# Kernel optimization log

Measured on AMD Instinct MI355X. Metric: run time of the kernel, lower is better.

Reference implementation:

```python
import jax, jax.numpy as jnp
import numpy as np
import math

B, N, CS, CZ, H, C, P, PV, NB = 1, 512, 384, 128, 12, 16, 4, 8, 64


def quat_to_rot(q):
    q = q / jnp.clip(jnp.linalg.norm(q, axis=-1, keepdims=True), 1e-8)
    w, x, y, z = q[..., 0], q[..., 1], q[..., 2], q[..., 3]
    return jnp.stack([
        w*w + x*x - y*y - z*z, 2*(x*y - w*z), 2*(x*z + w*y),
        2*(x*y + w*z), w*w - x*x + y*y - z*z, 2*(y*z - w*x),
        2*(x*z - w*y), 2*(y*z + w*x), w*w - x*x - y*y + z*z,
    ], axis=-1).reshape(q.shape[:-1] + (3, 3))


def setup_inputs() -> dict:
    key = jax.random.key(0)
    ks = jax.random.split(key, 28)
    def n(k, shape, sc=1.0):
        return jax.random.normal(k, shape, jnp.float32) * sc
    s = n(ks[0], (B, N, CS))
    z = n(ks[1], (B, N, N, CZ))
    translations = n(ks[2], (B, N, 3)) * 4.0  # spread distances over 0-32A bins
    rotations = quat_to_rot(n(ks[3], (B, N, 4)))  # valid SO(3) frames
    mask = jnp.ones((B, N), dtype=bool)
    inv = lambda fan: 1.0 / math.sqrt(fan)
    return {
        's': s, 'z': z, 'translations': translations, 'rotations': rotations, 'mask': mask,
        'Wq': n(ks[4], (CS, H*C), inv(CS)), 'bq': n(ks[5], (H*C,), 0.01),
        'Wk': n(ks[6], (CS, H*C), inv(CS)), 'bk': n(ks[7], (H*C,), 0.01),
        'Wv': n(ks[8], (CS, H*C), inv(CS)), 'bv': n(ks[9], (H*C,), 0.01),
        'Wqp': n(ks[10], (CS, H*P*3), inv(CS)), 'bqp': n(ks[11], (H*P*3,), 0.01),
        'Wkp': n(ks[12], (CS, H*P*3), inv(CS)), 'bkp': n(ks[13], (H*P*3,), 0.01),
        'Wvp': n(ks[14], (CS, H*PV*3), inv(CS)), 'bvp': n(ks[15], (H*PV*3,), 0.01),
        'Wb': n(ks[16], (CZ, H), inv(CZ)), 'bb': n(ks[17], (H,), 0.01),
        'dist_emb': n(ks[18], (NB, H), 0.02),
        'scale_logits': n(ks[19], (3, H), 0.1),
        'head_weights': jnp.abs(n(ks[20], (H,))) * 0.2 + 0.8,
        'Wout': n(ks[21], (H*(C + PV*4 + CZ), CS), inv(H*(C + PV*4 + CZ))),
        'bout': n(ks[22], (CS,), 0.01),
    }


def reference(s, z, translations, rotations, mask, Wq, bq, Wk, bk, Wv, bv,
              Wqp, bqp, Wkp, bkp, Wvp, bvp, Wb, bb, dist_emb, scale_logits,
              head_weights, Wout, bout):
    b, n, _ = s.shape
    q = (s @ Wq + bq).reshape(b, n, H, C)
    k = (s @ Wk + bk).reshape(b, n, H, C)
    v = (s @ Wv + bv).reshape(b, n, H, C)
    q_pts = (s @ Wqp + bqp).reshape(b, n, H, P, 3)
    k_pts = (s @ Wkp + bkp).reshape(b, n, H, P, 3)
    v_pts = (s @ Wvp + bvp).reshape(b, n, H, PV, 3)
    t = translations[:, :, None, None, :]
    q_g = jnp.einsum('bnij,bnhpj->bnhpi', rotations, q_pts) + t
    k_g = jnp.einsum('bnij,bnhpj->bnhpi', rotations, k_pts) + t
    v_g = jnp.einsum('bnij,bnhpj->bnhpi', rotations, v_pts) + t
    scalar_logits = jnp.einsum('bnhc,bmhc->bnmh', q, k) / math.sqrt(C)
    # squared point distances, summed over points p and coords i, via expansion
    q_sq = (q_g**2).sum((-1, -2))  # (b, n, h)
    k_sq = (k_g**2).sum((-1, -2))
    cross = jnp.einsum('bnhpi,bmhpi->bnmh', q_g, k_g)
    point_dist = q_sq[:, :, None, :] + k_sq[:, None, :, :] - 2.0 * cross
    point_logits = -0.5 * point_dist * head_weights
    pair_bias = z @ Wb + bb  # (b, n, m, h)
    pair_dist = jnp.linalg.norm(
        translations[:, :, None, :] - translations[:, None, :, :], axis=-1)
    edges = jnp.linspace(0.0, 32.0, NB + 1)
    bins = jnp.clip(jnp.searchsorted(edges, pair_dist, side='left') - 1, 0, NB - 1)
    dist_bias = dist_emb[bins]
    local = (pair_dist <= 5.0).astype(s.dtype)
    medium = ((pair_dist > 5.0) & (pair_dist <= 15.0)).astype(s.dtype)
    scales = jnp.stack([local, medium, jnp.ones_like(pair_dist)], axis=-1)
    per_head = jax.nn.softmax(scale_logits, axis=0)  # (3, h)
    multiscale = jnp.einsum('bnms,sh->bnmh', scales, per_head)
    logits = scalar_logits + point_logits + pair_bias + dist_bias + multiscale
    m2d = mask[:, :, None] & mask[:, None, :]
    logits = jnp.where(m2d[..., None], logits, -10000.0)
    attn = jax.nn.softmax(logits.astype(jnp.float32), axis=2).astype(s.dtype)
    out_scalar = jnp.einsum('bnmh,bmhc->bnhc', attn, v)
    out_pts_g = jnp.einsum('bnmh,bmhpi->bnhpi', attn, v_g)
    out_pts_l = jnp.einsum('bnji,bnhpj->bnhpi', rotations, out_pts_g - t)  # R^T x
    out_norms = jnp.linalg.norm(out_pts_l, axis=-1)  # (b, n, h, pv)
    pair_feat = jnp.einsum('bnmh,bnmc->bnhc', attn, z)
    feats = jnp.concatenate(
        [out_scalar, out_pts_l.reshape(b, n, H, PV * 3), out_norms, pair_feat],
        axis=-1).reshape(b, n, -1)
    return feats @ Wout + bout
```

## Files before the change

kernel.cpp:

```cpp
#include <hip/hip_runtime.h>
#include <math.h>

#define N   512
#define CS  384
#define CZ  128
#define H   12
#define C   16
#define P   4
#define PV  8
#define NB  64
#define KSP 528
#define QKD 28
#define QPAD 68
#define APAD 516

#define OFF_Q    0
#define OFF_K    98304
#define OFF_V    196608
#define OFF_QP   294912
#define OFF_KP   368640
#define OFF_VP   442368
#define OFF_QG   589824
#define OFF_KG   663552
#define OFF_VG   737280
#define OFF_QSQ  884736
#define OFF_KSQ  890880
#define OFF_LOG  897024
#define OFF_FEAT 4042752

__global__ __launch_bounds__(256) void k_proj(
    const float* __restrict__ s,
    const float* __restrict__ Wq,  const float* __restrict__ bq,
    const float* __restrict__ Wk,  const float* __restrict__ bk,
    const float* __restrict__ Wv,  const float* __restrict__ bv,
    const float* __restrict__ Wqp, const float* __restrict__ bqp,
    const float* __restrict__ Wkp, const float* __restrict__ bkp,
    const float* __restrict__ Wvp, const float* __restrict__ bvp,
    float* __restrict__ ws)
{
    __shared__ float s_s[16*388];
    __shared__ float part[4*16*68];
    const int tid = threadIdx.x;
    const int n0  = blockIdx.y * 16;
    const int cq  = tid & 15;
    const int rg  = (tid >> 4) & 3;
    const int ks  = tid >> 6;
    const int gc  = blockIdx.x * 64 + cq * 4;
    for (int i = tid; i < 16*384; i += 256) {
        int r = i / 384, c = i - r*384;
        s_s[r*388 + c] = s[(n0 + r)*384 + c];
    }
    __syncthreads();
    const float* W; int width; int lc;
    if      (gc < 192) { W=Wq;  width=192; lc=gc;     }
    else if (gc < 384) { W=Wk;  width=192; lc=gc-192; }
    else if (gc < 576) { W=Wv;  width=192; lc=gc-384; }
    else if (gc < 720) { W=Wqp; width=144; lc=gc-576; }
    else if (gc < 864) { W=Wkp; width=144; lc=gc-720; }
    else               { W=Wvp; width=288; lc=gc-864; }
    float acc[4][4] = {{0.f}};
    const float* wp   = W + lc + (size_t)(ks*96)*width;
    const float* srow = s_s + (rg*4)*388 + ks*96;
    #pragma unroll 4
    for (int kk = 0; kk < 96; kk++) {
        float4 w4 = *(const float4*)(wp + (size_t)kk*width);
        #pragma unroll
        for (int r = 0; r < 4; r++) {
            float sv = srow[r*388 + kk];
            acc[r][0] += sv*w4.x; acc[r][1] += sv*w4.y;
            acc[r][2] += sv*w4.z; acc[r][3] += sv*w4.w;
        }
    }
    #pragma unroll
    for (int r = 0; r < 4; r++)
        *(float4*)(part + (ks*16 + rg*4 + r)*68 + cq*4) =
            make_float4(acc[r][0], acc[r][1], acc[r][2], acc[r][3]);
    __syncthreads();
    {
        const int row = tid >> 4;
        float4 sum = *(const float4*)(part + (0*16 + row)*68 + cq*4);
        #pragma unroll
        for (int k2 = 1; k2 < 4; k2++) {
            float4 p = *(const float4*)(part + (k2*16 + row)*68 + cq*4);
            sum.x += p.x; sum.y += p.y; sum.z += p.z; sum.w += p.w;
        }
        const float* b; float* dst; int w2, lc2;
        if      (gc < 192) { b=bq;  w2=192; lc2=gc;     dst=ws+OFF_Q;  }
        else if (gc < 384) { b=bk;  w2=192; lc2=gc-192; dst=ws+OFF_K;  }
        else if (gc < 576) { b=bv;  w2=192; lc2=gc-384; dst=ws+OFF_V;  }
        else if (gc < 720) { b=bqp; w2=144; lc2=gc-576; dst=ws+OFF_QP; }
        else if (gc < 864) { b=bkp; w2=144; lc2=gc-720; dst=ws+OFF_KP; }
        else               { b=bvp; w2=288; lc2=gc-864; dst=ws+OFF_VP; }
        float4 b4 = *(const float4*)(b + lc2);
        sum.x += b4.x; sum.y += b4.y; sum.z += b4.z; sum.w += b4.w;
        *(float4*)(dst + (size_t)(n0+row)*w2 + lc2) = sum;
    }
}

__global__ __launch_bounds__(192) void k_frames(
    const float* __restrict__ rot, const float* __restrict__ trans,
    float* __restrict__ ws)
{
    int n = blockIdx.x, tid = threadIdx.x;
    __shared__ float R[9], T[3], qg_s[144], kg_s[144];
    if (tid < 9) R[tid] = rot[n*9 + tid];
    if (tid < 3) T[tid] = trans[n*3 + tid];
    __syncthreads();
    if (tid < 48) {
        const float* lp = ws + OFF_QP + n*144 + tid*3;
        float l0=lp[0], l1=lp[1], l2=lp[2];
        float* gp = ws + OFF_QG + n*144 + tid*3;
        for (int i=0;i<3;i++){ float g = R[i*3+0]*l0 + R[i*3+1]*l1 + R[i*3+2]*l2 + T[i]; gp[i]=g; qg_s[tid*3+i]=g; }
    } else if (tid < 96) {
        int u = tid-48;
        const float* lp = ws + OFF_KP + n*144 + u*3;
        float l0=lp[0], l1=lp[1], l2=lp[2];
        float* gp = ws + OFF_KG + n*144 + u*3;
        for (int i=0;i<3;i++){ float g = R[i*3+0]*l0 + R[i*3+1]*l1 + R[i*3+2]*l2 + T[i]; gp[i]=g; kg_s[u*3+i]=g; }
    } else {
        int u = tid-96;
        const float* lp = ws + OFF_VP + n*288 + u*3;
        float l0=lp[0], l1=lp[1], l2=lp[2];
        float* gp = ws + OFF_VG + n*288 + u*3;
        for (int i=0;i<3;i++){ float g = R[i*3+0]*l0 + R[i*3+1]*l1 + R[i*3+2]*l2 + T[i]; gp[i]=g; }
    }
    __syncthreads();
    if (tid < 12) {
        float a=0;
        for (int d=0; d<12; d++){ float x=qg_s[tid*12+d]; a+=x*x; }
        ws[OFF_QSQ + n*12 + tid]=a;
    } else if (tid < 24) {
        int h = tid-12; float a=0;
        for (int d=0; d<12; d++){ float x=kg_s[h*12+d]; a+=x*x; }
        ws[OFF_KSQ + n*12 + h]=a;
    }
}

__global__ __launch_bounds__(256) void k_qkpt(
    const float* __restrict__ head_weights, float* __restrict__ ws)
{
    __shared__ float qs[QKD*QPAD], ks[QKD*QPAD], qa[64], kb[64];
    const int tid = threadIdx.x;
    const int m0 = blockIdx.x * 64, n0 = blockIdx.y * 64, h = blockIdx.z;
    const float hw = head_weights[h];
    for (int idx = tid; idx < 64*16; idx += 256) {
        int r = idx >> 4, c = idx & 15;
        qs[c*QPAD + r] = ws[OFF_Q + (n0+r)*192 + h*16 + c] * 0.25f;
        ks[c*QPAD + r] = ws[OFF_K + (m0+r)*192 + h*16 + c];
    }
    for (int idx = tid; idx < 64*12; idx += 256) {
        int r = idx / 12, c = idx % 12;
        qs[(16+c)*QPAD + r] = ws[OFF_QG + (n0+r)*144 + h*12 + c] * hw;
        ks[(16+c)*QPAD + r] = ws[OFF_KG + (m0+r)*144 + h*12 + c];
    }
    for (int idx = tid; idx < 64; idx += 256) {
        qa[idx] = -0.5f * hw * ws[OFF_QSQ + (n0+idx)*12 + h];
        kb[idx] = -0.5f * hw * ws[OFF_KSQ + (m0+idx)*12 + h];
    }
    __syncthreads();
    const int tx = tid & 15, ty = tid >> 4;
    float acc[4][4] = {{0.f}};
    #pragma unroll 4
    for (int d = 0; d < QKD; d++) {
        float4 a = *(const float4*)(qs + d*QPAD + ty*4);
        float4 b = *(const float4*)(ks + d*QPAD + tx*4);
        const float* ap = &a.x; const float* bp = &b.x;
        #pragma unroll
        for (int i=0;i<4;i++)
            #pragma unroll
            for (int j=0;j<4;j++) acc[i][j] += ap[i]*bp[j];
    }
    #pragma unroll
    for (int i=0;i<4;i++) {
        float ai = qa[ty*4+i];
        float4 r;
        r.x = acc[i][0] + ai + kb[tx*4+0];
        r.y = acc[i][1] + ai + kb[tx*4+1];
        r.z = acc[i][2] + ai + kb[tx*4+2];
        r.w = acc[i][3] + ai + kb[tx*4+3];
        *(float4*)(ws + OFF_LOG + ((size_t)(n0+ty*4+i)*H + h)*N + m0 + tx*4) = r;
    }
}

__global__ __launch_bounds__(256) void k_attn_all(
    const float* __restrict__ z, const float* __restrict__ trans,
    const float* __restrict__ rot,
    const float* __restrict__ Wb, const float* __restrict__ bb,
    const float* __restrict__ dist_emb, const float* __restrict__ scale_logits,
    float* __restrict__ ws)
{
    __shared__ float attn_s[H*APAD];
    __shared__ float part[4*12*64];
    __shared__ float og_s[288];
    __shared__ float sprob[36];
    const int n = blockIdx.x, tid = threadIdx.x;
    const int lane = tid & 63, wave = tid >> 6;

    if (tid < 12) {
        float sa = scale_logits[tid], sb = scale_logits[12+tid], sc = scale_logits[24+tid];
        float mx = fmaxf(sa, fmaxf(sb, sc));
        float ea=__expf(sa-mx), eb=__expf(sb-mx), ec=__expf(sc-mx);
        float inv = 1.f/(ea+eb+ec);
        sprob[tid] = ea*inv; sprob[12+tid] = eb*inv; sprob[24+tid] = ec*inv;
    }

    const float4* asrc = (const float4*)(ws + OFF_LOG + (size_t)n*H*N);
    for (int i = tid; i < H*(N/4); i += 256) {
        int h = i >> 7, q = i & 127;
        *(float4*)(attn_s + h*APAD + q*4) = asrc[h*128 + q];
    }
    __syncthreads();

    const float tnx = trans[n*3+0], tny = trans[n*3+1], tnz = trans[n*3+2];
    const float4 bb0 = *(const float4*)(bb);
    const float4 bb1 = *(const float4*)(bb+4);
    const float4 bb2 = *(const float4*)(bb+8);
    for (int half = 0; half < 2; half++) {
        const int m = tid + half*256;
        float dx = tnx - trans[m*3+0];
        float dy = tny - trans[m*3+1];
        float dz = tnz - trans[m*3+2];
        float pd = sqrtf(dx*dx+dy*dy+dz*dz);
        int bin = (int)ceilf(2.f*pd) - 1;
        bin = bin < 0 ? 0 : (bin > NB-1 ? NB-1 : bin);
        const float4 de0 = *(const float4*)(dist_emb + bin*12);
        const float4 de1 = *(const float4*)(dist_emb + bin*12 + 4);
        const float4 de2 = *(const float4*)(dist_emb + bin*12 + 8);
        const int ssel = (pd <= 5.f) ? 0 : (pd <= 15.f ? 1 : -1);
        float4 a0, a1, a2;
        {
            float4 pc0 = *(const float4*)(sprob+24);
            float4 pc1 = *(const float4*)(sprob+28);
            float4 pc2 = *(const float4*)(sprob+32);
            a0.x = bb0.x + de0.x + pc0.x; a0.y = bb0.y + de0.y + pc0.y;
            a0.z = bb0.z + de0.z + pc0.z; a0.w = bb0.w + de0.w + pc0.w;
            a1.x = bb1.x + de1.x + pc1.x; a1.y = bb1.y + de1.y + pc1.y;
            a1.z = bb1.z + de1.z + pc1.z; a1.w = bb1.w + de1.w + pc1.w;
            a2.x = bb2.x + de2.x + pc2.x; a2.y = bb2.y + de2.y + pc2.y;
            a2.z = bb2.z + de2.z + pc2.z; a2.w = bb2.w + de2.w + pc2.w;
            if (ssel >= 0) {
                const float* sp = sprob + ssel*12;
                float4 p0 = *(const float4*)(sp);
                float4 p1 = *(const float4*)(sp+4);
                float4 p2 = *(const float4*)(sp+8);
                a0.x += p0.x; a0.y += p0.y; a0.z += p0.z; a0.w += p0.w;
                a1.x += p1.x; a1.y += p1.y; a1.z += p1.z; a1.w += p1.w;
                a2.x += p2.x; a2.y += p2.y; a2.z += p2.z; a2.w += p2.w;
            }
        }
        const float* zp = z + ((size_t)n*N + m)*CZ;
        #pragma unroll 2
        for (int c4 = 0; c4 < CZ/4; c4++) {
            float4 z4 = *(const float4*)(zp + c4*4);
            const float* zv = &z4.x;
            #pragma unroll
            for (int j=0; j<4; j++) {
                const float* wr = Wb + (c4*4+j)*12;
                float4 w0 = *(const float4*)(wr);
                float4 w1 = *(const float4*)(wr+4);
                float4 w2 = *(const float4*)(wr+8);
                float zj = zv[j];
                a0.x += zj*w0.x; a0.y += zj*w0.y; a0.z += zj*w0.z; a0.w += zj*w0.w;
                a1.x += zj*w1.x; a1.y += zj*w1.y; a1.z += zj*w1.z; a1.w += zj*w1.w;
                a2.x += zj*w2.x; a2.y += zj*w2.y; a2.z += zj*w2.z; a2.w += zj*w2.w;
            }
        }
        attn_s[0*APAD + m] += a0.x;  attn_s[1*APAD + m] += a0.y;
        attn_s[2*APAD + m] += a0.z;  attn_s[3*APAD + m] += a0.w;
        attn_s[4*APAD + m] += a1.x;  attn_s[5*APAD + m] += a1.y;
        attn_s[6*APAD + m] += a1.z;  attn_s[7*APAD + m] += a1.w;
        attn_s[8*APAD + m] += a2.x;  attn_s[9*APAD + m] += a2.y;
        attn_s[10*APAD + m] += a2.z; attn_s[11*APAD + m] += a2.w;
    }
    __syncthreads();

    for (int h = wave; h < H; h += 4) {
        float* row = attn_s + h*APAD;
        float v[8]; float mx = -1e30f;
        #pragma unroll
        for (int j=0;j<8;j++){ v[j]=row[lane + j*64]; mx = fmaxf(mx, v[j]); }
        #pragma unroll
        for (int off=32; off>0; off>>=1) mx = fmaxf(mx, __shfl_xor(mx, off, 64));
        float sum = 0.f;
        #pragma unroll
        for (int j=0;j<8;j++){ v[j]=__expf(v[j]-mx); sum += v[j]; }
        #pragma unroll
        for (int off=32; off>0; off>>=1) sum += __shfl_xor(sum, off, 64);
        float inv = 1.f/sum;
        #pragma unroll
        for (int j=0;j<8;j++) row[lane + j*64] = v[j]*inv;
    }
    __syncthreads();

    const int cq = tid & 15;
    const int ms = tid >> 4;
    for (int ch = 0; ch < 2; ch++) {
        const float* zb = z + (size_t)n*N*CZ + ch*64 + cq*4;
        float4 acc[12];
        #pragma unroll
        for (int h=0; h<12; h++) acc[h] = make_float4(0.f,0.f,0.f,0.f);
        const int r0 = ms*32;
        #pragma unroll 2
        for (int rq = 0; rq < 8; rq++) {
            const int r = r0 + rq*4;
            float4 z0 = *(const float4*)(zb + (size_t)(r+0)*CZ);
            float4 z1 = *(const float4*)(zb + (size_t)(r+1)*CZ);
            float4 z2 = *(const float4*)(zb + (size_t)(r+2)*CZ);
            float4 z3 = *(const float4*)(zb + (size_t)(r+3)*CZ);
            #pragma unroll
            for (int h=0; h<12; h++) {
                float4 a4 = *(const float4*)(attn_s + h*APAD + r);
                acc[h].x += a4.x*z0.x + a4.y*z1.x + a4.z*z2.x + a4.w*z3.x;
                acc[h].y += a4.x*z0.y + a4.y*z1.y + a4.z*z2.y + a4.w*z3.y;
                acc[h].z += a4.x*z0.z + a4.y*z1.z + a4.z*z2.z + a4.w*z3.z;
                acc[h].w += a4.x*z0.w + a4.y*z1.w + a4.z*z2.w + a4.w*z3.w;
            }
        }
        #pragma unroll
        for (int h=0; h<12; h++) {
            acc[h].x += __shfl_xor(acc[h].x, 16, 64); acc[h].y += __shfl_xor(acc[h].y, 16, 64);
            acc[h].z += __shfl_xor(acc[h].z, 16, 64); acc[h].w += __shfl_xor(acc[h].w, 16, 64);
            acc[h].x += __shfl_xor(acc[h].x, 32, 64); acc[h].y += __shfl_xor(acc[h].y, 32, 64);
            acc[h].z += __shfl_xor(acc[h].z, 32, 64); acc[h].w += __shfl_xor(acc[h].w, 32, 64);
        }
        if (lane < 16) {
            #pragma unroll
            for (int h=0; h<12; h++)
                *(float4*)(part + (wave*12 + h)*64 + lane*4) = acc[h];
        }
        __syncthreads();
        if (tid < 192) {
            const int h = tid >> 4, c4 = tid & 15;
            float4 s4 = *(const float4*)(part + (0*12 + h)*64 + c4*4);
            #pragma unroll
            for (int w=1; w<4; w++) {
                float4 p = *(const float4*)(part + (w*12 + h)*64 + c4*4);
                s4.x += p.x; s4.y += p.y; s4.z += p.z; s4.w += p.w;
            }
            *(float4*)(ws + OFF_FEAT + (size_t)n*2112 + h*176 + 48 + ch*64 + c4*4) = s4;
        }
        __syncthreads();
    }

    if (tid < 240) {
        const int col4 = (tid % 120) * 4;
        const int msA  = tid / 120;
        const float* aptr; int astride, ah;
        if (col4 < 192) { ah = col4 >> 4;        aptr = ws + OFF_V  + col4;       astride = 192; }
        else            { ah = (col4-192) / 24;  aptr = ws + OFF_VG + (col4-192); astride = 288; }
        const float4* arow = (const float4*)(attn_s + ah*APAD);
        float4 acc = {0.f,0.f,0.f,0.f};
        #pragma unroll 2
        for (int mq = msA*64; mq < msA*64 + 64; mq++) {
            float4 a4 = arow[mq];
            const float* vp = aptr + (size_t)mq*4*astride;
            float4 v0 = *(const float4*)(vp);
            float4 v1 = *(const float4*)(vp + astride);
            float4 v2 = *(const float4*)(vp + 2*astride);
            float4 v3 = *(const float4*)(vp + 3*astride);
            acc.x += a4.x*v0.x + a4.y*v1.x + a4.z*v2.x + a4.w*v3.x;
            acc.y += a4.x*v0.y + a4.y*v1.y + a4.z*v2.y + a4.w*v3.y;
            acc.z += a4.x*v0.z + a4.y*v1.z + a4.z*v2.z + a4.w*v3.z;
            acc.w += a4.x*v0.w + a4.y*v1.w + a4.z*v2.w + a4.w*v3.w;
        }
        *(float4*)(part + tid*4) = acc;
    }
    __syncthreads();
    if (tid < 120) {
        const int col4 = tid * 4;
        float4 a = *(const float4*)(part + tid*4);
        float4 b = *(const float4*)(part + (tid+120)*4);
        a.x += b.x; a.y += b.y; a.z += b.z; a.w += b.w;
        if (col4 < 192) {
            const int ah = col4 >> 4;
            *(float4*)(ws + OFF_FEAT + (size_t)n*2112 + ah*176 + (col4 & 15)) = a;
        } else {
            *(float4*)(og_s + (col4 - 192)) = a;
        }
    }
    __syncthreads();
    if (tid < 96) {
        const int h = tid >> 3, p = tid & 7;
        float g0 = og_s[h*24 + p*3 + 0] - trans[n*3+0];
        float g1 = og_s[h*24 + p*3 + 1] - trans[n*3+1];
        float g2 = og_s[h*24 + p*3 + 2] - trans[n*3+2];
        const float* R = rot + n*9;
        float* fdst = ws + OFF_FEAT + (size_t)n*2112 + h*176;
        float nsq = 0.f;
        #pragma unroll
        for (int i=0;i<3;i++){
            float l = R[0*3+i]*g0 + R[1*3+i]*g1 + R[2*3+i]*g2;
            fdst[16 + p*3 + i] = l;
            nsq += l*l;
        }
        fdst[40 + p] = sqrtf(nsq);
    }
}

__global__ __launch_bounds__(384) void k_bias(
    const float* __restrict__ bout, float* __restrict__ out)
{
    out[(size_t)blockIdx.x*CS + threadIdx.x] = bout[threadIdx.x];
}

__global__ __launch_bounds__(256) void k_out(
    const float* __restrict__ Wout, const float* __restrict__ ws,
    float* __restrict__ out)
{
    __shared__ float f_s[16*KSP];
    __shared__ float part[4*16*68];
    const int tid = threadIdx.x;
    const int n0  = blockIdx.y * 16;
    const int k0  = blockIdx.z * KSP;
    const int cq  = tid & 15;
    const int rg  = (tid >> 4) & 3;
    const int ks  = tid >> 6;
    const int col = blockIdx.x * 64 + cq * 4;
    for (int i = tid; i < 16*KSP; i += 256) {
        int r = i / KSP, c = i - r*KSP;
        f_s[i] = ws[OFF_FEAT + (size_t)(n0 + r)*2112 + k0 + c];
    }
    __syncthreads();
    float acc[4][4] = {{0.f}};
    const float* wp = Wout + (size_t)(k0 + ks*132)*CS + col;
    const float* f0 = f_s + (rg*4)*KSP + ks*132;
    #pragma unroll 4
    for (int kk = 0; kk < 132; kk++) {
        float4 w4 = *(const float4*)(wp + (size_t)kk*CS);
        #pragma unroll
        for (int r = 0; r < 4; r++) {
            float fv = f0[r*KSP + kk];
            acc[r][0] += fv*w4.x; acc[r][1] += fv*w4.y;
            acc[r][2] += fv*w4.z; acc[r][3] += fv*w4.w;
        }
    }
    #pragma unroll
    for (int r = 0; r < 4; r++)
        *(float4*)(part + (ks*16 + rg*4 + r)*68 + cq*4) =
            make_float4(acc[r][0], acc[r][1], acc[r][2], acc[r][3]);
    __syncthreads();
    {
        const int row = tid >> 4;
        float4 s = *(const float4*)(part + (0*16 + row)*68 + cq*4);
        #pragma unroll
        for (int k2 = 1; k2 < 4; k2++) {
            float4 p = *(const float4*)(part + (k2*16 + row)*68 + cq*4);
            s.x += p.x; s.y += p.y; s.z += p.z; s.w += p.w;
        }
        float* o = out + (size_t)(n0+row)*CS + col;
        atomicAdd(o+0, s.x); atomicAdd(o+1, s.y);
        atomicAdd(o+2, s.z); atomicAdd(o+3, s.w);
    }
}

extern "C" void kernel_launch(void* const* d_in, const int* in_sizes, int n_in,
                              void* d_out, int out_size, void* d_ws, size_t ws_size,
                              hipStream_t stream) {
    const float* s     = (const float*)d_in[0];
    const float* z     = (const float*)d_in[1];
    const float* trans = (const float*)d_in[2];
    const float* rot   = (const float*)d_in[3];
    const float* Wq  = (const float*)d_in[5];  const float* bq  = (const float*)d_in[6];
    const float* Wk  = (const float*)d_in[7];  const float* bk  = (const float*)d_in[8];
    const float* Wv  = (const float*)d_in[9];  const float* bv  = (const float*)d_in[10];
    const float* Wqp = (const float*)d_in[11]; const float* bqp = (const float*)d_in[12];
    const float* Wkp = (const float*)d_in[13]; const float* bkp = (const float*)d_in[14];
    const float* Wvp = (const float*)d_in[15]; const float* bvp = (const float*)d_in[16];
    const float* Wb  = (const float*)d_in[17]; const float* bb  = (const float*)d_in[18];
    const float* dist_emb     = (const float*)d_in[19];
    const float* scale_logits = (const float*)d_in[20];
    const float* head_weights = (const float*)d_in[21];
    const float* Wout = (const float*)d_in[22]; const float* bout = (const float*)d_in[23];
    float* out = (float*)d_out;
    float* ws  = (float*)d_ws;

    k_proj<<<dim3(18, 32), 256, 0, stream>>>(s, Wq,bq, Wk,bk, Wv,bv, Wqp,bqp, Wkp,bkp, Wvp,bvp, ws);
    k_frames<<<N, 192, 0, stream>>>(rot, trans, ws);
    k_qkpt<<<dim3(8, 8, 12), 256, 0, stream>>>(head_weights, ws);
    k_attn_all<<<N, 256, 0, stream>>>(z, trans, rot, Wb, bb, dist_emb, scale_logits, ws);
    k_bias<<<N, CS, 0, stream>>>(bout, out);
    k_out<<<dim3(6, 32, 4), 256, 0, stream>>>(Wout, ws, out);
}
```

Baseline: 348.3 us.

## Split fused attention kernel into bias-softmax and two-role attention-matmul kernels

The single per-row attention kernel is split in two. The first computes the pair bias and softmax and writes the probabilities back to the workspace. The second runs with two blocks per row: one does the attention-weighted pair-feature reduction over z, the other does the value and point aggregation. This roughly doubles the block count in the aggregation phase to improve occupancy and overlap. In exchange it adds an extra kernel launch and a write-then-reread of the attention matrix through global memory.

```diff
diff --git a/kernel.cpp b/kernel.cpp
--- a/kernel.cpp
+++ b/kernel.cpp
@@ -182,16 +182,13 @@
     }
 }
 
-__global__ __launch_bounds__(256) void k_attn_all(
+__global__ __launch_bounds__(256) void k_biassm(
     const float* __restrict__ z, const float* __restrict__ trans,
-    const float* __restrict__ rot,
     const float* __restrict__ Wb, const float* __restrict__ bb,
     const float* __restrict__ dist_emb, const float* __restrict__ scale_logits,
     float* __restrict__ ws)
 {
     __shared__ float attn_s[H*APAD];
-    __shared__ float part[4*12*64];
-    __shared__ float og_s[288];
     __shared__ float sprob[36];
     const int n = blockIdx.x, tid = threadIdx.x;
     const int lane = tid & 63, wave = tid >> 6;
@@ -204,10 +201,10 @@
         sprob[tid] = ea*inv; sprob[12+tid] = eb*inv; sprob[24+tid] = ec*inv;
     }
 
-    const float4* asrc = (const float4*)(ws + OFF_LOG + (size_t)n*H*N);
+    float4* abase = (float4*)(ws + OFF_LOG + (size_t)n*H*N);
     for (int i = tid; i < H*(N/4); i += 256) {
         int h = i >> 7, q = i & 127;
-        *(float4*)(attn_s + h*APAD + q*4) = asrc[h*128 + q];
+        *(float4*)(attn_s + h*APAD + q*4) = abase[h*128 + q];
     }
     __syncthreads();
 
@@ -232,12 +229,12 @@
             float4 pc0 = *(const float4*)(sprob+24);
             float4 pc1 = *(const float4*)(sprob+28);
             float4 pc2 = *(const float4*)(sprob+32);
-            a0.x = bb0.x + de0.x + pc0.x; a0.y = bb0.y + de0.y + pc0.y;
-            a0.z = bb0.z + de0.z + pc0.z; a0.w = bb0.w + de0.w + pc0.w;
-            a1.x = bb1.x + de1.x + pc1.x; a1.y = bb1.y + de1.y + pc1.y;
-            a1.z = bb1.z + de1.z + pc1.z; a1.w = bb1.w + de1.w + pc1.w;
-            a2.x = bb2.x + de2.x + pc2.x; a2.y = bb2.y + de2.y + pc2.y;
-            a2.z = bb2.z + de2.z + pc2.z; a2.w = bb2.w + de2.w + pc2.w;
+            a0.x = bb0.x+de0.x+pc0.x; a0.y = bb0.y+de0.y+pc0.y;
+            a0.z = bb0.z+de0.z+pc0.z; a0.w = bb0.w+de0.w+pc0.w;
+            a1.x = bb1.x+de1.x+pc1.x; a1.y = bb1.y+de1.y+pc1.y;
+            a1.z = bb1.z+de1.z+pc1.z; a1.w = bb1.w+de1.w+pc1.w;
+            a2.x = bb2.x+de2.x+pc2.x; a2.y = bb2.y+de2.y+pc2.y;
+            a2.z = bb2.z+de2.z+pc2.z; a2.w = bb2.w+de2.w+pc2.w;
             if (ssel >= 0) {
                 const float* sp = sprob + ssel*12;
                 float4 p0 = *(const float4*)(sp);
@@ -291,109 +288,133 @@
         for (int j=0;j<8;j++) row[lane + j*64] = v[j]*inv;
     }
     __syncthreads();
-
-    const int cq = tid & 15;
-    const int ms = tid >> 4;
-    for (int ch = 0; ch < 2; ch++) {
-        const float* zb = z + (size_t)n*N*CZ + ch*64 + cq*4;
-        float4 acc[12];
-        #pragma unroll
-        for (int h=0; h<12; h++) acc[h] = make_float4(0.f,0.f,0.f,0.f);
-        const int r0 = ms*32;
-        #pragma unroll 2
-        for (int rq = 0; rq < 8; rq++) {
-            const int r = r0 + rq*4;
-            float4 z0 = *(const float4*)(zb + (size_t)(r+0)*CZ);
-            float4 z1 = *(const float4*)(zb + (size_t)(r+1)*CZ);
-            float4 z2 = *(const float4*)(zb + (size_t)(r+2)*CZ);
-            float4 z3 = *(const float4*)(zb + (size_t)(r+3)*CZ);
+    for (int i = tid; i < H*(N/4); i += 256) {
+        int h = i >> 7, q = i & 127;
+        abase[h*128 + q] = *(const float4*)(attn_s + h*APAD + q*4);
+    }
+}
+
+__global__ __launch_bounds__(256) void k_attnmm(
+    const float* __restrict__ z, const float* __restrict__ trans,
+    const float* __restrict__ rot, float* __restrict__ ws)
+{
+    __shared__ float attn_s[H*APAD];
+    __shared__ float part[4*12*64];
+    __shared__ float og_s[288];
+    const int n = blockIdx.x, role = blockIdx.y, tid = threadIdx.x;
+    const int lane = tid & 63, wave = tid >> 6;
+
+    const float4* asrc = (const float4*)(ws + OFF_LOG + (size_t)n*H*N);
+    for (int i = tid; i < H*(N/4); i += 256) {
+        int h = i >> 7, q = i & 127;
+        *(float4*)(attn_s + h*APAD + q*4) = asrc[h*128 + q];
+    }
+    __syncthreads();
+
+    if (role == 0) {
+        const int cq = tid & 15;
+        const int ms = tid >> 4;
+        for (int ch = 0; ch < 2; ch++) {
+            const float* zb = z + (size_t)n*N*CZ + ch*64 + cq*4;
+            float4 acc[12];
+            #pragma unroll
+            for (int h=0; h<12; h++) acc[h] = make_float4(0.f,0.f,0.f,0.f);
+            const int r0 = ms*32;
+            #pragma unroll 2
+            for (int rq = 0; rq < 8; rq++) {
+                const int r = r0 + rq*4;
+                float4 z0 = *(const float4*)(zb + (size_t)(r+0)*CZ);
+                float4 z1 = *(const float4*)(zb + (size_t)(r+1)*CZ);
+                float4 z2 = *(const float4*)(zb + (size_t)(r+2)*CZ);
+                float4 z3 = *(const float4*)(zb + (size_t)(r+3)*CZ);
+                #pragma unroll
+                for (int h=0; h<12; h++) {
+                    float4 a4 = *(const float4*)(attn_s + h*APAD + r);
+                    acc[h].x += a4.x*z0.x + a4.y*z1.x + a4.z*z2.x + a4.w*z3.x;
+                    acc[h].y += a4.x*z0.y + a4.y*z1.y + a4.z*z2.y + a4.w*z3.y;
+                    acc[h].z += a4.x*z0.z + a4.y*z1.z + a4.z*z2.z + a4.w*z3.z;
+                    acc[h].w += a4.x*z0.w + a4.y*z1.w + a4.z*z2.w + a4.w*z3.w;
+                }
+            }
             #pragma unroll
             for (int h=0; h<12; h++) {
-                float4 a4 = *(const float4*)(attn_s + h*APAD + r);
-                acc[h].x += a4.x*z0.x + a4.y*z1.x + a4.z*z2.x + a4.w*z3.x;
-                acc[h].y += a4.x*z0.y + a4.y*z1.y + a4.z*z2.y + a4.w*z3.y;
-                acc[h].z += a4.x*z0.z + a4.y*z1.z + a4.z*z2.z + a4.w*z3.z;
-                acc[h].w += a4.x*z0.w + a4.y*z1.w + a4.z*z2.w + a4.w*z3.w;
-            }
-        }
-        #pragma unroll
-        for (int h=0; h<12; h++) {
-            acc[h].x += __shfl_xor(acc[h].x, 16, 64); acc[h].y += __shfl_xor(acc[h].y, 16, 64);
-            acc[h].z += __shfl_xor(acc[h].z, 16, 64); acc[h].w += __shfl_xor(acc[h].w, 16, 64);
-            acc[h].x += __shfl_xor(acc[h].x, 32, 64); acc[h].y += __shfl_xor(acc[h].y, 32, 64);
-            acc[h].z += __shfl_xor(acc[h].z, 32, 64); acc[h].w += __shfl_xor(acc[h].w, 32, 64);
-        }
-        if (lane < 16) {
+                acc[h].x += __shfl_xor(acc[h].x, 16, 64); acc[h].y += __shfl_xor(acc[h].y, 16, 64);
+                acc[h].z += __shfl_xor(acc[h].z, 16, 64); acc[h].w += __shfl_xor(acc[h].w, 16, 64);
+                acc[h].x += __shfl_xor(acc[h].x, 32, 64); acc[h].y += __shfl_xor(acc[h].y, 32, 64);
+                acc[h].z += __shfl_xor(acc[h].z, 32, 64); acc[h].w += __shfl_xor(acc[h].w, 32, 64);
+            }
+            if (lane < 16) {
+                #pragma unroll
+                for (int h=0; h<12; h++)
+                    *(float4*)(part + (wave*12 + h)*64 + lane*4) = acc[h];
+            }
+            __syncthreads();
+            if (tid < 192) {
+                const int h = tid >> 4, c4 = tid & 15;
+                float4 s4 = *(const float4*)(part + (0*12 + h)*64 + c4*4);
+                #pragma unroll
+                for (int w=1; w<4; w++) {
+                    float4 p = *(const float4*)(part + (w*12 + h)*64 + c4*4);
+                    s4.x += p.x; s4.y += p.y; s4.z += p.z; s4.w += p.w;
+                }
+                *(float4*)(ws + OFF_FEAT + (size_t)n*2112 + h*176 + 48 + ch*64 + c4*4) = s4;
+            }
+            __syncthreads();
+        }
+    } else {
+        if (tid < 240) {
+            const int col4 = (tid % 120) * 4;
+            const int msA  = tid / 120;
+            const float* aptr; int astride, ah;
+            if (col4 < 192) { ah = col4 >> 4;        aptr = ws + OFF_V  + col4;       astride = 192; }
+            else            { ah = (col4-192) / 24;  aptr = ws + OFF_VG + (col4-192); astride = 288; }
+            const float4* arow = (const float4*)(attn_s + ah*APAD);
+            float4 acc = {0.f,0.f,0.f,0.f};
+            #pragma unroll 2
+            for (int mq = msA*64; mq < msA*64 + 64; mq++) {
+                float4 a4 = arow[mq];
+                const float* vp = aptr + (size_t)mq*4*astride;
+                float4 v0 = *(const float4*)(vp);
+                float4 v1 = *(const float4*)(vp + astride);
+                float4 v2 = *(const float4*)(vp + 2*astride);
+                float4 v3 = *(const float4*)(vp + 3*astride);
+                acc.x += a4.x*v0.x + a4.y*v1.x + a4.z*v2.x + a4.w*v3.x;
+                acc.y += a4.x*v0.y + a4.y*v1.y + a4.z*v2.y + a4.w*v3.y;
+                acc.z += a4.x*v0.z + a4.y*v1.z + a4.z*v2.z + a4.w*v3.z;
+                acc.w += a4.x*v0.w + a4.y*v1.w + a4.z*v2.w + a4.w*v3.w;
+            }
+            *(float4*)(part + tid*4) = acc;
+        }
+        __syncthreads();
+        if (tid < 120) {
+            const int col4 = tid * 4;
+            float4 a = *(const float4*)(part + tid*4);
+            float4 b = *(const float4*)(part + (tid+120)*4);
+            a.x += b.x; a.y += b.y; a.z += b.z; a.w += b.w;
+            if (col4 < 192) {
+                const int ah = col4 >> 4;
+                *(float4*)(ws + OFF_FEAT + (size_t)n*2112 + ah*176 + (col4 & 15)) = a;
+            } else {
+                *(float4*)(og_s + (col4 - 192)) = a;
+            }
+        }
+        __syncthreads();
+        if (tid < 96) {
+            const int h = tid >> 3, p = tid & 7;
+            float g0 = og_s[h*24 + p*3 + 0] - trans[n*3+0];
+            float g1 = og_s[h*24 + p*3 + 1] - trans[n*3+1];
+            float g2 = og_s[h*24 + p*3 + 2] - trans[n*3+2];
+            const float* R = rot + n*9;
+            float* fdst = ws + OFF_FEAT + (size_t)n*2112 + h*176;
+            float nsq = 0.f;
             #pragma unroll
-            for (int h=0; h<12; h++)
-                *(float4*)(part + (wave*12 + h)*64 + lane*4) = acc[h];
-        }
-        __syncthreads();
-        if (tid < 192) {
-            const int h = tid >> 4, c4 = tid & 15;
-            float4 s4 = *(const float4*)(part + (0*12 + h)*64 + c4*4);
-            #pragma unroll
-            for (int w=1; w<4; w++) {
-                float4 p = *(const float4*)(part + (w*12 + h)*64 + c4*4);
-                s4.x += p.x; s4.y += p.y; s4.z += p.z; s4.w += p.w;
-            }
-            *(float4*)(ws + OFF_FEAT + (size_t)n*2112 + h*176 + 48 + ch*64 + c4*4) = s4;
-        }
-        __syncthreads();
-    }
-
-    if (tid < 240) {
-        const int col4 = (tid % 120) * 4;
-        const int msA  = tid / 120;
-        const float* aptr; int astride, ah;
-        if (col4 < 192) { ah = col4 >> 4;        aptr = ws + OFF_V  + col4;       astride = 192; }
-        else            { ah = (col4-192) / 24;  aptr = ws + OFF_VG + (col4-192); astride = 288; }
-        const float4* arow = (const float4*)(attn_s + ah*APAD);
-        float4 acc = {0.f,0.f,0.f,0.f};
-        #pragma unroll 2
-        for (int mq = msA*64; mq < msA*64 + 64; mq++) {
-            float4 a4 = arow[mq];
-            const float* vp = aptr + (size_t)mq*4*astride;
-            float4 v0 = *(const float4*)(vp);
-            float4 v1 = *(const float4*)(vp + astride);
-            float4 v2 = *(const float4*)(vp + 2*astride);
-            float4 v3 = *(const float4*)(vp + 3*astride);
-            acc.x += a4.x*v0.x + a4.y*v1.x + a4.z*v2.x + a4.w*v3.x;
-            acc.y += a4.x*v0.y + a4.y*v1.y + a4.z*v2.y + a4.w*v3.y;
-            acc.z += a4.x*v0.z + a4.y*v1.z + a4.z*v2.z + a4.w*v3.z;
-            acc.w += a4.x*v0.w + a4.y*v1.w + a4.z*v2.w + a4.w*v3.w;
-        }
-        *(float4*)(part + tid*4) = acc;
-    }
-    __syncthreads();
-    if (tid < 120) {
-        const int col4 = tid * 4;
-        float4 a = *(const float4*)(part + tid*4);
-        float4 b = *(const float4*)(part + (tid+120)*4);
-        a.x += b.x; a.y += b.y; a.z += b.z; a.w += b.w;
-        if (col4 < 192) {
-            const int ah = col4 >> 4;
-            *(float4*)(ws + OFF_FEAT + (size_t)n*2112 + ah*176 + (col4 & 15)) = a;
-        } else {
-            *(float4*)(og_s + (col4 - 192)) = a;
-        }
-    }
-    __syncthreads();
-    if (tid < 96) {
-        const int h = tid >> 3, p = tid & 7;
-        float g0 = og_s[h*24 + p*3 + 0] - trans[n*3+0];
-        float g1 = og_s[h*24 + p*3 + 1] - trans[n*3+1];
-        float g2 = og_s[h*24 + p*3 + 2] - trans[n*3+2];
-        const float* R = rot + n*9;
-        float* fdst = ws + OFF_FEAT + (size_t)n*2112 + h*176;
-        float nsq = 0.f;
-        #pragma unroll
-        for (int i=0;i<3;i++){
-            float l = R[0*3+i]*g0 + R[1*3+i]*g1 + R[2*3+i]*g2;
-            fdst[16 + p*3 + i] = l;
-            nsq += l*l;
-        }
-        fdst[40 + p] = sqrtf(nsq);
+            for (int i=0;i<3;i++){
+                float l = R[0*3+i]*g0 + R[1*3+i]*g1 + R[2*3+i]*g2;
+                fdst[16 + p*3 + i] = l;
+                nsq += l*l;
+            }
+            fdst[40 + p] = sqrtf(nsq);
+        }
     }
 }
 
@@ -477,7 +498,8 @@
     k_proj<<<dim3(18, 32), 256, 0, stream>>>(s, Wq,bq, Wk,bk, Wv,bv, Wqp,bqp, Wkp,bkp, Wvp,bvp, ws);
     k_frames<<<N, 192, 0, stream>>>(rot, trans, ws);
     k_qkpt<<<dim3(8, 8, 12), 256, 0, stream>>>(head_weights, ws);
-    k_attn_all<<<N, 256, 0, stream>>>(z, trans, rot, Wb, bb, dist_emb, scale_logits, ws);
+    k_biassm<<<N, 256, 0, stream>>>(z, trans, Wb, bb, dist_emb, scale_logits, ws);
+    k_attnmm<<<dim3(N, 2), 256, 0, stream>>>(z, trans, rot, ws);
     k_bias<<<N, CS, 0, stream>>>(bout, out);
     k_out<<<dim3(6, 32, 4), 256, 0, stream>>>(Wout, ws, out);
 }
```

After: 350.2 us. No clear change (+0.6%).
